# Performance work log

Measured on AMD Instinct MI355X. Metric: run time of the kernel, lower is better.

## Reference

```python
import jax, jax.numpy as jnp
import numpy as np

B, S, LD, Hh, Ww = 64, 32, 16, 32, 18
D, NH, HD, FF, L = 512, 8, 64, 2048, 6
IN = LD * Hh * Ww  # 9216
EPS = 1e-5


def setup_inputs() -> dict:
    key = jax.random.key(0)
    ks = jax.random.split(key, 8)
    p = lambda k, s: jax.random.normal(k, s, jnp.float32) * 0.02
    return {
        "x": jax.random.normal(ks[0], (B, S, LD, Hh, Ww), jnp.float32),
        "inp_w": p(ks[1], (D, IN)), "inp_b": jnp.zeros((D,), jnp.float32),
        "in_proj_w": p(ks[2], (L, 3 * D, D)), "in_proj_b": jnp.zeros((L, 3 * D), jnp.float32),
        "out_w": p(ks[3], (L, D, D)), "out_b": jnp.zeros((L, D), jnp.float32),
        "ln1_w": jnp.ones((L, D), jnp.float32), "ln1_b": jnp.zeros((L, D), jnp.float32),
        "ln2_w": jnp.ones((L, D), jnp.float32), "ln2_b": jnp.zeros((L, D), jnp.float32),
        "ff1_w": p(ks[4], (L, FF, D)), "ff1_b": jnp.zeros((L, FF), jnp.float32),
        "ff2_w": p(ks[5], (L, D, FF)), "ff2_b": jnp.zeros((L, D), jnp.float32),
        "outp_w": p(ks[6], (IN, D)), "outp_b": jnp.zeros((IN,), jnp.float32),
    }


def _layernorm(x, w, b):
    mu = jnp.mean(x, -1, keepdims=True)
    var = jnp.mean(jnp.square(x - mu), -1, keepdims=True)
    return (x - mu) * jax.lax.rsqrt(var + EPS) * w + b


def _rope(x, cos, sin):
    # x: [B,S,NH,HD]; torchtune interleaved-pair rotation, rope applied BEFORE qk projection
    x2 = x.reshape(*x.shape[:-1], HD // 2, 2)
    x0, x1 = x2[..., 0], x2[..., 1]
    c = cos[None, :, None, :]
    s = sin[None, :, None, :]
    out = jnp.stack([x0 * c - x1 * s, x1 * c + x0 * s], axis=-1)
    return out.reshape(x.shape)


def reference(x, inp_w, inp_b, in_proj_w, in_proj_b, out_w, out_b,
              ln1_w, ln1_b, ln2_w, ln2_b, ff1_w, ff1_b, ff2_w, ff2_b,
              outp_w, outp_b):
    b, s = x.shape[0], x.shape[1]
    h = x.reshape(b, s, IN) @ inp_w.T + inp_b  # [B,S,D]

    theta = 1.0 / (10000.0 ** (jnp.arange(0, HD, 2, dtype=jnp.float32) / HD))
    ang = jnp.arange(s, dtype=jnp.float32)[:, None] * theta  # [S, HD/2]
    cos, sin = jnp.cos(ang), jnp.sin(ang)
    mask = jnp.triu(jnp.full((s, s), -jnp.inf, jnp.float32), k=1)  # causal additive mask
    scale = 1.0 / np.sqrt(HD)

    for i in range(L):
        # RoPE on full hidden state (pre-projection), used for q and k; v uses unrotated h
        hr = _rope(h.reshape(b, s, NH, HD), cos, sin).reshape(b, s, D)
        wq, wk, wv = in_proj_w[i, :D], in_proj_w[i, D:2 * D], in_proj_w[i, 2 * D:]
        bq, bk, bv = in_proj_b[i, :D], in_proj_b[i, D:2 * D], in_proj_b[i, 2 * D:]
        q = (hr @ wq.T + bq).reshape(b, s, NH, HD)
        k = (hr @ wk.T + bk).reshape(b, s, NH, HD)
        v = (h @ wv.T + bv).reshape(b, s, NH, HD)
        scores = jnp.einsum('bqhd,bkhd->bhqk', q, k) * scale + mask
        attn = jax.nn.softmax(scores, axis=-1)
        ctx = jnp.einsum('bhqk,bkhd->bqhd', attn, v).reshape(b, s, D)
        sa = ctx @ out_w[i].T + out_b[i]
        h = _layernorm(h + sa, ln1_w[i], ln1_b[i])  # post-norm (norm_first=False)
        ff = jax.nn.gelu(h @ ff1_w[i].T + ff1_b[i], approximate=False) @ ff2_w[i].T + ff2_b[i]
        h = _layernorm(h + ff, ln2_w[i], ln2_b[i])

    out = h @ outp_w.T + outp_b
    return out.reshape(b, s, LD, Hh, Ww)
```

## Files before the change

### kernel.cpp

```cpp
#include <hip/hip_runtime.h>
#include <hip/hip_bf16.h>
#include <math.h>


typedef __attribute__((ext_vector_type(8))) short bf16x8;
typedef __attribute__((ext_vector_type(4))) short bf16x4;
typedef __attribute__((ext_vector_type(8))) float f32x8;
typedef __attribute__((ext_vector_type(4))) float f32x4;

#define LN_EPS 1e-5f

__device__ inline float bf2f(__hip_bfloat16 v) { return __bfloat162float(v); }
__device__ inline __hip_bfloat16 f2bf(float f) { return __float2bfloat16(f); }

__device__ __forceinline__ void gload_lds16(const __hip_bfloat16* g, __hip_bfloat16* l) {
    __builtin_amdgcn_global_load_lds(
        (const __attribute__((address_space(1))) unsigned*)g,
        (__attribute__((address_space(3))) unsigned*)l, 16, 0, 0);
}

__device__ __forceinline__ void sync_tile() {
    asm volatile("s_waitcnt vmcnt(0) lgkmcnt(0)" ::: "memory");
    __builtin_amdgcn_s_barrier();
    asm volatile("" ::: "memory");
}

__device__ __forceinline__ void sync_lds() {
    asm volatile("s_waitcnt lgkmcnt(0)" ::: "memory");
    __builtin_amdgcn_s_barrier();
    asm volatile("" ::: "memory");
}

struct CvtSeg { const float* src; __hip_bfloat16* dst; };
struct CvtArgs { CvtSeg seg[16]; long cum[17]; };

__global__ __launch_bounds__(256) void convert_all(CvtArgs a, long total8,
                                                   float* __restrict__ rtab) {
    if (blockIdx.x == 0) {
#pragma unroll
        for (int it = 0; it < 4; ++it) {
            const int t = it * 256 + threadIdx.x;
            const int s = t >> 5, p = t & 31;
            const float theta = powf(10000.f, -(float)p / 32.f);
            float sn, cs;
            sincosf((float)s * theta, &sn, &cs);
            rtab[t * 2] = cs;
            rtab[t * 2 + 1] = sn;
        }
    }
    const long st = (long)gridDim.x * 256;
    for (long i = (long)blockIdx.x * 256 + threadIdx.x; i < total8; i += 2 * st) {
        int s1 = 0;
        while (i >= a.cum[s1 + 1]) ++s1;
        const long o1 = i - a.cum[s1];
        const f32x8 x1 = *((const f32x8*)a.seg[s1].src + o1);

        const long j = i + st;
        if (j < total8) {
            int s2 = s1;
            while (j >= a.cum[s2 + 1]) ++s2;
            const long o2 = j - a.cum[s2];
            const f32x8 x2 = *((const f32x8*)a.seg[s2].src + o2);

            union { bf16x8 v; __hip_bfloat16 b[8]; } u1, u2;
#pragma unroll
            for (int t = 0; t < 8; ++t) { u1.b[t] = f2bf(x1[t]); u2.b[t] = f2bf(x2[t]); }
            *((bf16x8*)a.seg[s1].dst + o1) = u1.v;
            *((bf16x8*)a.seg[s2].dst + o2) = u2.v;
        } else {
            union { bf16x8 v; __hip_bfloat16 b[8]; } u1;
#pragma unroll
            for (int t = 0; t < 8; ++t) u1.b[t] = f2bf(x1[t]);
            *((bf16x8*)a.seg[s1].dst + o1) = u1.v;
        }
    }
}

template<int BM, int BN, int EPI, int OUT, int AMODE, int SWZ, int PIPE>
__global__ __launch_bounds__(256) void gemm_bt(
    const void* __restrict__ Araw, int bn_split,
    const float* __restrict__ rtab,
    const __hip_bfloat16* __restrict__ W,
    const __hip_bfloat16* __restrict__ bias,
    void* __restrict__ Cv,
    int M, int N, int Ktot, int KC)
{
    constexpr int FM = BM / 32, FN = BN / 32;
    constexpr int CPT_A = BM / 32, CPT_B = BN / 32;
    constexpr bool REGSTAGE = (AMODE == 3 || AMODE == 4);
    constexpr int NBUF = (PIPE && !REGSTAGE) ? 2 : 1;
    __shared__ __align__(16) __hip_bfloat16 sA[NBUF][BM * 64];
    __shared__ __align__(16) __hip_bfloat16 sB[NBUF][BN * 64];

    const int tid = threadIdx.x, lane = tid & 63, wave = tid >> 6;
    const int wr = wave >> 1, wc = wave & 1;
    const int lr = lane & 15, lk = lane >> 4;

    int bm, bn, zz;
    if (SWZ == 0) {
        const int nbm = gridDim.x, nbn = gridDim.y;
        const int nwg = nbm * nbn;
        const int orig = blockIdx.y * nbm + blockIdx.x;
        const int q8 = nwg >> 3, r8 = nwg & 7;
        const int xcd = orig & 7, loc = orig >> 3;
        const int f = (xcd < r8 ? xcd * (q8 + 1) : r8 * (q8 + 1) + (xcd - r8) * q8) + loc;
        bm = f % nbm; bn = f / nbm; zz = blockIdx.z;
    } else {
        const int bid = blockIdx.x;
        const int xcd = bid & 7, loc = bid >> 3;
        const int nbn = N / BN;
        const int per = (gridDim.x >> 3) / nbn;
        bn = loc % nbn;
        const int gid = xcd * per + loc / nbn;
        bm = gid % (M / BM); zz = gid / (M / BM);
    }
    const int kbeg = zz * KC, kend = kbeg + KC;
    const bool dorot = (AMODE == 2 || AMODE == 4) && (bn < bn_split);

    const __hip_bfloat16* Ab = (const __hip_bfloat16*)Araw + (long)bm * BM * Ktot;
    const float*          Af = (const float*)Araw + (long)bm * BM * Ktot;
    const __hip_bfloat16* Wb = W + (long)bn * BN * Ktot;

    f32x4 acc[FM][FN];
#pragma unroll
    for (int i = 0; i < FM; ++i)
#pragma unroll
        for (int j = 0; j < FN; ++j) acc[i][j] = (f32x4){0.f, 0.f, 0.f, 0.f};

    f32x8  aregf[CPT_A];
    bf16x8 aregb[CPT_A];
    f32x8  csreg[CPT_A];
    bf16x8 bregb[REGSTAGE ? CPT_B : 1];

    auto stageA_g = [&](int buf, int k0) {
#pragma unroll
        for (int c = 0; c < CPT_A; ++c) {
            const int ch = tid + c * 256, row = ch >> 3, co = ch & 7;
            gload_lds16(&Ab[(long)row * Ktot + k0 + ((co ^ (row & 7)) * 8)],
                        (__hip_bfloat16*)((char*)&sA[buf][0] + ch * 16));
        }
    };
    auto stageB_g = [&](int buf, int k0) {
#pragma unroll
        for (int c = 0; c < CPT_B; ++c) {
            const int ch = tid + c * 256, row = ch >> 3, co = ch & 7;
            gload_lds16(&Wb[(long)row * Ktot + k0 + ((co ^ (row & 7)) * 8)],
                        (__hip_bfloat16*)((char*)&sB[buf][0] + ch * 16));
        }
    };
    auto issueA = [&](int k0) {
#pragma unroll
        for (int c = 0; c < CPT_A; ++c) {
            const int ch = tid + c * 256, row = ch >> 3, co = ch & 7;
            if (AMODE == 1 || AMODE == 3)
                aregf[c] = *(const f32x8*)&Af[(long)row * Ktot + k0 + co * 8];
            if (AMODE == 2 || AMODE == 4) {
                aregb[c] = *(const bf16x8*)&Ab[(long)row * Ktot + k0 + co * 8];
                if (dorot)
                    csreg[c] = *(const f32x8*)&rtab[((bm * BM + row) & 31) * 64 + co * 8];
            }
        }
        if (REGSTAGE) {
#pragma unroll
            for (int c = 0; c < CPT_B; ++c) {
                const int ch = tid + c * 256, row = ch >> 3, co = ch & 7;
                bregb[c] = *(const bf16x8*)&Wb[(long)row * Ktot + k0 + co * 8];
            }
        }
    };
    auto writeA = [&](int buf) {
#pragma unroll
        for (int c = 0; c < CPT_A; ++c) {
            const int ch = tid + c * 256, row = ch >> 3, co = ch & 7;
            union { bf16x8 v; __hip_bfloat16 b[8]; } t;
            if (AMODE == 1 || AMODE == 3) {
#pragma unroll
                for (int j = 0; j < 8; ++j) t.b[j] = f2bf(aregf[c][j]);
            } else {
                t.v = aregb[c];
                if (dorot) {
#pragma unroll
                    for (int qd = 0; qd < 4; ++qd) {
                        const float c_ = csreg[c][qd * 2], sn = csreg[c][qd * 2 + 1];
                        const float x0 = bf2f(t.b[2 * qd]);
                        const float x1 = bf2f(t.b[2 * qd + 1]);
                        t.b[2 * qd]     = f2bf(x0 * c_ - x1 * sn);
                        t.b[2 * qd + 1] = f2bf(x1 * c_ + x0 * sn);
                    }
                }
            }
            *(bf16x8*)((char*)&sA[buf][0] + row * 128 + ((co ^ (row & 7)) << 4)) = t.v;
        }
        if (REGSTAGE) {
#pragma unroll
            for (int c = 0; c < CPT_B; ++c) {
                const int ch = tid + c * 256, row = ch >> 3, co = ch & 7;
                *(bf16x8*)((char*)&sB[buf][0] + row * 128 + ((co ^ (row & 7)) << 4)) = bregb[c];
            }
        }
    };
    auto compute = [&](int buf) {
        bf16x8 af[2][FM], bfr[2][FN];
#pragma unroll
        for (int ks = 0; ks < 2; ++ks) {
#pragma unroll
            for (int i = 0; i < FM; ++i) {
                const int row = wr * (BM / 2) + i * 16 + lr;
                const int co = ks * 4 + lk;
                af[ks][i] = *(const bf16x8*)((const char*)&sA[buf][0] + row * 128 +
                                             ((co ^ (row & 7)) << 4));
            }
#pragma unroll
            for (int j = 0; j < FN; ++j) {
                const int row = wc * (BN / 2) + j * 16 + lr;
                const int co = ks * 4 + lk;
                bfr[ks][j] = *(const bf16x8*)((const char*)&sB[buf][0] + row * 128 +
                                              ((co ^ (row & 7)) << 4));
            }
        }
#pragma unroll
        for (int ks = 0; ks < 2; ++ks)
#pragma unroll
            for (int i = 0; i < FM; ++i)
#pragma unroll
                for (int j = 0; j < FN; ++j)
                    acc[i][j] = __builtin_amdgcn_mfma_f32_16x16x32_bf16(
                        af[ks][i], bfr[ks][j], acc[i][j], 0, 0, 0);
    };

    if (REGSTAGE) {
        issueA(kbeg);
        for (int k0 = kbeg; k0 < kend; k0 += 64) {
            if (k0 > kbeg) __builtin_amdgcn_s_barrier();
            writeA(0);
            sync_lds();
            if (k0 + 64 < kend) issueA(k0 + 64);
            compute(0);
        }
    } else if (PIPE == 0) {
        if (AMODE != 0) issueA(kbeg);
        for (int k0 = kbeg; k0 < kend; k0 += 64) {
            if (k0 > kbeg) __builtin_amdgcn_s_barrier();
            if (AMODE == 0) stageA_g(0, k0);
            stageB_g(0, k0);
            if (AMODE != 0) writeA(0);
            sync_tile();
            if (AMODE != 0 && k0 + 64 < kend) issueA(k0 + 64);
            compute(0);
        }
    } else {
        if (AMODE == 0) stageA_g(0, kbeg); else issueA(kbeg);
        stageB_g(0, kbeg);
        if (AMODE != 0) writeA(0);
        sync_tile();
        int cur = 0;
        for (int k0 = kbeg; k0 < kend; k0 += 64) {
            const bool hn = (k0 + 64 < kend);
            if (hn) {
                if (AMODE == 0) stageA_g(cur ^ 1, k0 + 64); else issueA(k0 + 64);
                stageB_g(cur ^ 1, k0 + 64);
            }
            compute(cur);
            if (hn) {
                if (AMODE != 0) writeA(cur ^ 1);
                sync_tile();
            }
            cur ^= 1;
        }
    }

    const int row0 = bm * BM + wr * (BM / 2);
    const int col0 = bn * BN + wc * (BN / 2);
    if (OUT == 1) {
        float* Cp = (float*)Cv + (long)zz * M * N;
#pragma unroll
        for (int i = 0; i < FM; ++i)
#pragma unroll
            for (int j = 0; j < FN; ++j) {
                const int col = col0 + j * 16 + lr;
#pragma unroll
                for (int r = 0; r < 4; ++r)
                    Cp[(long)(row0 + i * 16 + lk * 4 + r) * N + col] = acc[i][j][r];
            }
    } else {
#pragma unroll
        for (int i = 0; i < FM; ++i)
#pragma unroll
            for (int j = 0; j < FN; ++j) {
                const int col = col0 + j * 16 + lr;
                const float bv = bf2f(bias[col]);
#pragma unroll
                for (int r = 0; r < 4; ++r) {
                    const int row = row0 + i * 16 + lk * 4 + r;
                    float v = acc[i][j][r] + bv;
                    if (EPI == 1) v = 0.5f * v * (1.0f + erff(v * 0.70710678118654752f));
                    const long idx = (long)row * N + col;
                    if (OUT == 2) ((float*)Cv)[idx] = v;
                    else          ((__hip_bfloat16*)Cv)[idx] = f2bf(v);
                }
            }
    }
}

template<int SK>
__global__ __launch_bounds__(256) void sk_reduce(
    const float* __restrict__ part, const __hip_bfloat16* __restrict__ bias,
    __hip_bfloat16* __restrict__ out)
{
    const long MN = 2048L * 512;
    const long i4 = ((long)blockIdx.x * 256 + threadIdx.x) * 4;
    f32x4 s = (f32x4){0.f, 0.f, 0.f, 0.f};
#pragma unroll
    for (int z = 0; z < SK; ++z) s += *(const f32x4*)&part[z * MN + i4];
    const int col = (int)(i4 & 511);
    union { bf16x4 v; __hip_bfloat16 b[4]; } o;
#pragma unroll
    for (int j = 0; j < 4; ++j) o.b[j] = f2bf(s[j] + bf2f(bias[col + j]));
    *(bf16x4*)&out[i4] = o.v;
}

template<int SK>
__global__ __launch_bounds__(256) void skred_add_ln(
    const float* __restrict__ part, const __hip_bfloat16* __restrict__ bias,
    const __hip_bfloat16* __restrict__ resid,
    const __hip_bfloat16* __restrict__ w, const __hip_bfloat16* __restrict__ b,
    __hip_bfloat16* __restrict__ out)
{
    const long MN = 2048L * 512;
    const int wave = threadIdx.x >> 6, lane = threadIdx.x & 63;
    const long row = (long)blockIdx.x * 4 + wave;
    const long base = row * 512 + lane * 8;

    f32x8 acc = *(const f32x8*)&part[base];
#pragma unroll
    for (int z = 1; z < SK; ++z) acc += *(const f32x8*)&part[z * MN + base];

    union { bf16x8 v; __hip_bfloat16 b[8]; } ur, uo;
    ur.v = *(const bf16x8*)&resid[base];

    float x[8];
    float s = 0.f, s2 = 0.f;
#pragma unroll
    for (int j = 0; j < 8; ++j) {
        const int col = lane * 8 + j;
        x[j] = acc[j] + bf2f(bias[col]) + bf2f(ur.b[j]);
        s += x[j];
        s2 += x[j] * x[j];
    }
#pragma unroll
    for (int off = 32; off; off >>= 1) {
        s  += __shfl_xor(s, off);
        s2 += __shfl_xor(s2, off);
    }
    const float mu = s * (1.f / 512.f);
    const float var = s2 * (1.f / 512.f) - mu * mu;
    const float rs = rsqrtf(var + LN_EPS);
#pragma unroll
    for (int j = 0; j < 8; ++j) {
        const int col = lane * 8 + j;
        uo.b[j] = f2bf((x[j] - mu) * rs * bf2f(w[col]) + bf2f(b[col]));
    }
    *(bf16x8*)&out[base] = uo.v;
}

__global__ __launch_bounds__(256) void attn_mfma(
    const __hip_bfloat16* __restrict__ qkv, __hip_bfloat16* __restrict__ ctx)
{
    __shared__ __align__(16) __hip_bfloat16 sP[4][32 * 32];
    __shared__ __align__(16) __hip_bfloat16 sVT[4][64 * 32];

    const int wave = threadIdx.x >> 6, lane = threadIdx.x & 63;
    const int bh = blockIdx.x * 4 + wave;
    const int b = bh >> 3, head = bh & 7;
    const long tok0 = (long)b * 32;
    const int lr = lane & 15, lk = lane >> 4;

    const __hip_bfloat16* Qb = qkv + tok0 * 1536 + head * 64;
    const __hip_bfloat16* Kb = Qb + 512;
    const __hip_bfloat16* Vb = Qb + 1024;

#pragma unroll
    for (int t = 0; t < 4; ++t) {
        const int c = lane + t * 64, row = c >> 3, d0 = (c & 7) * 8;
        union { bf16x8 v; __hip_bfloat16 e[8]; } u;
        u.v = *(const bf16x8*)&Vb[(long)row * 1536 + d0];
#pragma unroll
        for (int e = 0; e < 8; ++e) sVT[wave][(d0 + e) * 32 + row] = u.e[e];
    }

    f32x4 sc[2][2];
#pragma unroll
    for (int i = 0; i < 2; ++i)
#pragma unroll
        for (int j = 0; j < 2; ++j) sc[i][j] = (f32x4){0.f, 0.f, 0.f, 0.f};
#pragma unroll
    for (int ks = 0; ks < 2; ++ks) {
        bf16x8 aq[2], bk[2];
#pragma unroll
        for (int i = 0; i < 2; ++i)
            aq[i] = *(const bf16x8*)&Qb[(long)(i * 16 + lr) * 1536 + ks * 32 + lk * 8];
#pragma unroll
        for (int j = 0; j < 2; ++j)
            bk[j] = *(const bf16x8*)&Kb[(long)(j * 16 + lr) * 1536 + ks * 32 + lk * 8];
#pragma unroll
        for (int i = 0; i < 2; ++i)
#pragma unroll
            for (int j = 0; j < 2; ++j)
                sc[i][j] = __builtin_amdgcn_mfma_f32_16x16x32_bf16(aq[i], bk[j], sc[i][j], 0, 0, 0);
    }

    float p[2][2][4], inv[2][4];
#pragma unroll
    for (int i = 0; i < 2; ++i) {
#pragma unroll
        for (int r = 0; r < 4; ++r) {
            const int row = i * 16 + lk * 4 + r;
            float m = -3.0e38f;
#pragma unroll
            for (int j = 0; j < 2; ++j) {
                const int col = j * 16 + lr;
                const float v = (col <= row) ? sc[i][j][r] * 0.125f : -3.0e38f;
                p[i][j][r] = v;
                m = fmaxf(m, v);
            }
#pragma unroll
            for (int off = 1; off < 16; off <<= 1)
                m = fmaxf(m, __shfl_xor(m, off));
            float l = 0.f;
#pragma unroll
            for (int j = 0; j < 2; ++j) {
                p[i][j][r] = expf(p[i][j][r] - m);
                l += p[i][j][r];
            }
#pragma unroll
            for (int off = 1; off < 16; off <<= 1)
                l += __shfl_xor(l, off);
            inv[i][r] = 1.f / l;
        }
    }

#pragma unroll
    for (int i = 0; i < 2; ++i)
#pragma unroll
        for (int j = 0; j < 2; ++j)
#pragma unroll
            for (int r = 0; r < 4; ++r)
                sP[wave][(i * 16 + lk * 4 + r) * 32 + j * 16 + lr] = f2bf(p[i][j][r]);

    bf16x8 pa[2], vb[4];
#pragma unroll
    for (int i = 0; i < 2; ++i)
        pa[i] = *(const bf16x8*)&sP[wave][(i * 16 + lr) * 32 + lk * 8];
#pragma unroll
    for (int j = 0; j < 4; ++j)
        vb[j] = *(const bf16x8*)&sVT[wave][(j * 16 + lr) * 32 + lk * 8];

    f32x4 o[2][4];
#pragma unroll
    for (int i = 0; i < 2; ++i)
#pragma unroll
        for (int j = 0; j < 4; ++j) {
            o[i][j] = (f32x4){0.f, 0.f, 0.f, 0.f};
            o[i][j] = __builtin_amdgcn_mfma_f32_16x16x32_bf16(pa[i], vb[j], o[i][j], 0, 0, 0);
        }

#pragma unroll
    for (int i = 0; i < 2; ++i)
#pragma unroll
        for (int j = 0; j < 4; ++j) {
            const int col = j * 16 + lr;
#pragma unroll
            for (int r = 0; r < 4; ++r) {
                const int row = i * 16 + lk * 4 + r;
                ctx[(tok0 + row) * 512 + head * 64 + col] = f2bf(o[i][j][r] * inv[i][r]);
            }
        }
}

extern "C" void kernel_launch(void* const* d_in, const int* in_sizes, int n_in,
                              void* d_out, int out_size, void* d_ws, size_t ws_size,
                              hipStream_t stream)
{
    const int M = 2048;
    __hip_bfloat16* wts = (__hip_bfloat16*)d_ws;

    const long O_INPW   = 0;
    const long O_INPROJ = 4718592;
    const long O_OUTW   = 9437184;
    const long O_FF1    = 11010048;
    const long O_FF2    = 17301504;
    const long O_OUTPW  = 23592960;
    const long O_INPB   = 28311552;
    const long O_INPROJB= 28312064;
    const long O_OUTB   = 28321280;
    const long O_LN1W   = 28324352;
    const long O_LN1B   = 28327424;
    const long O_LN2W   = 28330496;
    const long O_LN2B   = 28333568;
    const long O_FF1B   = 28336640;
    const long O_FF2B   = 28348928;
    const long O_OUTPB  = 28352000;
    const long O_ACT    = 28361216;

    __hip_bfloat16* h   = wts + O_ACT;
    __hip_bfloat16* ht  = h   + (long)M * 512;
    __hip_bfloat16* qkv = ht  + (long)M * 512;
    __hip_bfloat16* ctx = qkv + (long)M * 1536;
    __hip_bfloat16* ffh = ctx + (long)M * 512;
    float* rtab = (float*)(ffh + (long)M * 2048);
    float* skpart = (float*)((__hip_bfloat16*)rtab + 4096);

    const int  cidx[16] = {1, 3, 5, 11, 13, 15, 2, 4, 6, 7, 8, 9, 10, 12, 14, 16};
    const long coff[16] = {O_INPW, O_INPROJ, O_OUTW, O_FF1, O_FF2, O_OUTPW,
                           O_INPB, O_INPROJB, O_OUTB, O_LN1W, O_LN1B, O_LN2W,
                           O_LN2B, O_FF1B, O_FF2B, O_OUTPB};
    const long csz[16]  = {4718592, 4718592, 1572864, 6291456, 6291456, 4718592,
                           512, 9216, 3072, 3072, 3072, 3072, 3072, 12288, 3072, 9216};
    CvtArgs ca;
    long cum = 0;
    for (int s = 0; s < 16; ++s) {
        ca.seg[s].src = (const float*)d_in[cidx[s]];
        ca.seg[s].dst = wts + coff[s];
        ca.cum[s] = cum;
        cum += csz[s] / 8;
    }
    ca.cum[16] = cum;
    convert_all<<<2048, 256, 0, stream>>>(ca, cum, rtab);

    gemm_bt<64, 256, 0, 1, 3, 1, 0><<<512, 256, 0, stream>>>(
        d_in[0], 0, rtab, wts + O_INPW, wts + O_INPB, skpart, M, 512, 9216, 1152);
    sk_reduce<8><<<1024, 256, 0, stream>>>(skpart, wts + O_INPB, h);

    for (int i = 0; i < 6; ++i) {
        const __hip_bfloat16* wqkv = wts + O_INPROJ + (long)i * 1536 * 512;
        const __hip_bfloat16* bqkv = wts + O_INPROJB + i * 1536;

        gemm_bt<64, 128, 0, 0, 4, 0, 0><<<dim3(32, 12), 256, 0, stream>>>(
            h, 8, rtab, wqkv, bqkv, qkv, M, 1536, 512, 512);
        attn_mfma<<<128, 256, 0, stream>>>(qkv, ctx);
        gemm_bt<64, 64, 0, 1, 4, 0, 0><<<dim3(32, 8, 2), 256, 0, stream>>>(
            ctx, 0, rtab, wts + O_OUTW + (long)i * 512 * 512, wts + O_OUTB + i * 512,
            skpart, M, 512, 512, 256);
        skred_add_ln<2><<<512, 256, 0, stream>>>(
            skpart, wts + O_OUTB + i * 512, h,
            wts + O_LN1W + i * 512, wts + O_LN1B + i * 512, ht);
        gemm_bt<64, 128, 1, 0, 4, 0, 0><<<dim3(32, 16), 256, 0, stream>>>(
            ht, 0, rtab, wts + O_FF1 + (long)i * 2048 * 512, wts + O_FF1B + i * 2048,
            ffh, M, 2048, 512, 512);
        gemm_bt<64, 128, 0, 1, 4, 0, 0><<<dim3(32, 4, 4), 256, 0, stream>>>(
            ffh, 0, rtab, wts + O_FF2 + (long)i * 512 * 2048, wts + O_FF2B + i * 512,
            skpart, M, 512, 2048, 512);
        skred_add_ln<4><<<512, 256, 0, stream>>>(
            skpart, wts + O_FF2B + i * 512, ht,
            wts + O_LN2W + i * 512, wts + O_LN2B + i * 512, h);
    }

    gemm_bt<128, 128, 0, 2, 4, 0, 0><<<dim3(16, 72), 256, 0, stream>>>(
        h, 0, rtab, wts + O_OUTPW, wts + O_OUTPB, d_out, M, 9216, 512, 512);
}
```

Before: 458.4 us.

## Overlap remaining weight conversion with input-projection GEMM in one launch

Splits the fp32-to-bf16 weight conversion so that only the input-projection weight, its bias and the RoPE table are converted up front. The other layer weights are converted by extra workgroups appended to a specialized split-K input-projection GEMM kernel, so that conversion traffic runs alongside the large GEMM. The generic GEMM template is also trimmed to its register-staged path, dropping the unused LDS-direct and double-buffer variants. The risk is that the conversion blocks compete with the GEMM for bandwidth and CUs, and the first kernel now does a smaller job.

```diff
diff --git a/kernel.cpp b/kernel.cpp
--- a/kernel.cpp
+++ b/kernel.cpp
@@ -32,10 +32,13 @@
 }
 
 struct CvtSeg { const float* src; __hip_bfloat16* dst; };
-struct CvtArgs { CvtSeg seg[16]; long cum[17]; };
-
-__global__ __launch_bounds__(256) void convert_all(CvtArgs a, long total8,
-                                                   float* __restrict__ rtab) {
+struct CvtArgs14 { CvtSeg seg[14]; long cum[15]; };
+
+__global__ __launch_bounds__(256) void convert_pre(
+    const float* __restrict__ inpw_f, __hip_bfloat16* __restrict__ inpw_b,
+    const float* __restrict__ inpb_f, __hip_bfloat16* __restrict__ inpb_b,
+    float* __restrict__ rtab)
+{
     if (blockIdx.x == 0) {
 #pragma unroll
         for (int it = 0; it < 4; ++it) {
@@ -47,33 +50,176 @@
             rtab[t * 2] = cs;
             rtab[t * 2 + 1] = sn;
         }
-    }
+        if (threadIdx.x < 64) {
+            const long o = threadIdx.x;
+            const f32x8 x = *((const f32x8*)inpb_f + o);
+            union { bf16x8 v; __hip_bfloat16 b[8]; } u;
+#pragma unroll
+            for (int t = 0; t < 8; ++t) u.b[t] = f2bf(x[t]);
+            *((bf16x8*)inpb_b + o) = u.v;
+        }
+    }
+    const long total8 = 4718592 / 8;
     const long st = (long)gridDim.x * 256;
     for (long i = (long)blockIdx.x * 256 + threadIdx.x; i < total8; i += 2 * st) {
-        int s1 = 0;
-        while (i >= a.cum[s1 + 1]) ++s1;
-        const long o1 = i - a.cum[s1];
-        const f32x8 x1 = *((const f32x8*)a.seg[s1].src + o1);
-
+        const f32x8 x1 = *((const f32x8*)inpw_f + i);
         const long j = i + st;
         if (j < total8) {
-            int s2 = s1;
-            while (j >= a.cum[s2 + 1]) ++s2;
-            const long o2 = j - a.cum[s2];
-            const f32x8 x2 = *((const f32x8*)a.seg[s2].src + o2);
-
+            const f32x8 x2 = *((const f32x8*)inpw_f + j);
             union { bf16x8 v; __hip_bfloat16 b[8]; } u1, u2;
 #pragma unroll
             for (int t = 0; t < 8; ++t) { u1.b[t] = f2bf(x1[t]); u2.b[t] = f2bf(x2[t]); }
-            *((bf16x8*)a.seg[s1].dst + o1) = u1.v;
-            *((bf16x8*)a.seg[s2].dst + o2) = u2.v;
+            *((bf16x8*)inpw_b + i) = u1.v;
+            *((bf16x8*)inpw_b + j) = u2.v;
         } else {
             union { bf16x8 v; __hip_bfloat16 b[8]; } u1;
 #pragma unroll
             for (int t = 0; t < 8; ++t) u1.b[t] = f2bf(x1[t]);
-            *((bf16x8*)a.seg[s1].dst + o1) = u1.v;
-        }
-    }
+            *((bf16x8*)inpw_b + i) = u1.v;
+        }
+    }
+}
+
+__global__ __launch_bounds__(256) void inproj_conv(
+    const float* __restrict__ Xf,
+    const __hip_bfloat16* __restrict__ Wall,
+    float* __restrict__ part,
+    CvtArgs14 ca, long total8)
+{
+    __shared__ __align__(16) __hip_bfloat16 sA[64 * 64];
+    __shared__ __align__(16) __hip_bfloat16 sB[256 * 64];
+
+    const int tid = threadIdx.x;
+
+    if (blockIdx.x >= 512) {
+        const long st = 2048L * 256;
+        for (long i = (long)(blockIdx.x - 512) * 256 + tid; i < total8; i += 2 * st) {
+            int s1 = 0;
+            while (i >= ca.cum[s1 + 1]) ++s1;
+            const long o1 = i - ca.cum[s1];
+            const f32x8 x1 = *((const f32x8*)ca.seg[s1].src + o1);
+            const long j = i + st;
+            if (j < total8) {
+                int s2 = s1;
+                while (j >= ca.cum[s2 + 1]) ++s2;
+                const long o2 = j - ca.cum[s2];
+                const f32x8 x2 = *((const f32x8*)ca.seg[s2].src + o2);
+                union { bf16x8 v; __hip_bfloat16 b[8]; } u1, u2;
+#pragma unroll
+                for (int t = 0; t < 8; ++t) { u1.b[t] = f2bf(x1[t]); u2.b[t] = f2bf(x2[t]); }
+                *((bf16x8*)ca.seg[s1].dst + o1) = u1.v;
+                *((bf16x8*)ca.seg[s2].dst + o2) = u2.v;
+            } else {
+                union { bf16x8 v; __hip_bfloat16 b[8]; } u1;
+#pragma unroll
+                for (int t = 0; t < 8; ++t) u1.b[t] = f2bf(x1[t]);
+                *((bf16x8*)ca.seg[s1].dst + o1) = u1.v;
+            }
+        }
+        return;
+    }
+
+    const int lane = tid & 63, wave = tid >> 6;
+    const int wr = wave >> 1, wc = wave & 1;
+    const int lr = lane & 15, lk = lane >> 4;
+
+    const int bid = blockIdx.x;
+    const int xcd = bid & 7, loc = bid >> 3;
+    const int bn = loc & 1;
+    const int gid = xcd * 32 + (loc >> 1);
+    const int bm = gid & 31;
+    const int zz = gid >> 5;
+    const int kbeg = zz * 1152, kend = kbeg + 1152;
+
+    const float* Ab = Xf + (long)bm * 64 * 9216;
+    const __hip_bfloat16* Wb = Wall + (long)bn * 256 * 9216;
+
+    f32x4 acc[2][8];
+#pragma unroll
+    for (int i = 0; i < 2; ++i)
+#pragma unroll
+        for (int j = 0; j < 8; ++j) acc[i][j] = (f32x4){0.f, 0.f, 0.f, 0.f};
+
+    f32x8  aregf[2];
+    bf16x8 bregb[8];
+
+    auto issueA = [&](int k0) {
+#pragma unroll
+        for (int c = 0; c < 2; ++c) {
+            const int ch = tid + c * 256, row = ch >> 3, co = ch & 7;
+            aregf[c] = *(const f32x8*)&Ab[(long)row * 9216 + k0 + co * 8];
+        }
+#pragma unroll
+        for (int c = 0; c < 8; ++c) {
+            const int ch = tid + c * 256, row = ch >> 3, co = ch & 7;
+            bregb[c] = *(const bf16x8*)&Wb[(long)row * 9216 + k0 + co * 8];
+        }
+    };
+    auto writeA = [&]() {
+#pragma unroll
+        for (int c = 0; c < 2; ++c) {
+            const int ch = tid + c * 256, row = ch >> 3, co = ch & 7;
+            union { bf16x8 v; __hip_bfloat16 b[8]; } t;
+#pragma unroll
+            for (int j = 0; j < 8; ++j) t.b[j] = f2bf(aregf[c][j]);
+            *(bf16x8*)((char*)sA + row * 128 + ((co ^ (row & 7)) << 4)) = t.v;
+        }
+#pragma unroll
+        for (int c = 0; c < 8; ++c) {
+            const int ch = tid + c * 256, row = ch >> 3, co = ch & 7;
+            *(bf16x8*)((char*)sB + row * 128 + ((co ^ (row & 7)) << 4)) = bregb[c];
+        }
+    };
+    auto compute = [&]() {
+        bf16x8 af[2][2], bfr[2][8];
+#pragma unroll
+        for (int ks = 0; ks < 2; ++ks) {
+#pragma unroll
+            for (int i = 0; i < 2; ++i) {
+                const int row = wr * 32 + i * 16 + lr;
+                const int co = ks * 4 + lk;
+                af[ks][i] = *(const bf16x8*)((const char*)sA + row * 128 +
+                                             ((co ^ (row & 7)) << 4));
+            }
+#pragma unroll
+            for (int j = 0; j < 8; ++j) {
+                const int row = wc * 128 + j * 16 + lr;
+                const int co = ks * 4 + lk;
+                bfr[ks][j] = *(const bf16x8*)((const char*)sB + row * 128 +
+                                              ((co ^ (row & 7)) << 4));
+            }
+        }
+#pragma unroll
+        for (int ks = 0; ks < 2; ++ks)
+#pragma unroll
+            for (int i = 0; i < 2; ++i)
+#pragma unroll
+                for (int j = 0; j < 8; ++j)
+                    acc[i][j] = __builtin_amdgcn_mfma_f32_16x16x32_bf16(
+                        af[ks][i], bfr[ks][j], acc[i][j], 0, 0, 0);
+    };
+
+    issueA(kbeg);
+    for (int k0 = kbeg; k0 < kend; k0 += 64) {
+        if (k0 > kbeg) __builtin_amdgcn_s_barrier();
+        writeA();
+        sync_lds();
+        if (k0 + 64 < kend) issueA(k0 + 64);
+        compute();
+    }
+
+    float* Cp = part + (long)zz * 2048 * 512;
+    const int row0 = bm * 64 + wr * 32;
+    const int col0 = bn * 256 + wc * 128;
+#pragma unroll
+    for (int i = 0; i < 2; ++i)
+#pragma unroll
+        for (int j = 0; j < 8; ++j) {
+            const int col = col0 + j * 16 + lr;
+#pragma unroll
+            for (int r = 0; r < 4; ++r)
+                Cp[(long)(row0 + i * 16 + lk * 4 + r) * 512 + col] = acc[i][j][r];
+        }
 }
 
 template<int BM, int BN, int EPI, int OUT, int AMODE, int SWZ, int PIPE>
@@ -87,38 +233,25 @@
 {
     constexpr int FM = BM / 32, FN = BN / 32;
     constexpr int CPT_A = BM / 32, CPT_B = BN / 32;
-    constexpr bool REGSTAGE = (AMODE == 3 || AMODE == 4);
-    constexpr int NBUF = (PIPE && !REGSTAGE) ? 2 : 1;
-    __shared__ __align__(16) __hip_bfloat16 sA[NBUF][BM * 64];
-    __shared__ __align__(16) __hip_bfloat16 sB[NBUF][BN * 64];
+    __shared__ __align__(16) __hip_bfloat16 sA[BM * 64];
+    __shared__ __align__(16) __hip_bfloat16 sB[BN * 64];
 
     const int tid = threadIdx.x, lane = tid & 63, wave = tid >> 6;
     const int wr = wave >> 1, wc = wave & 1;
     const int lr = lane & 15, lk = lane >> 4;
 
-    int bm, bn, zz;
-    if (SWZ == 0) {
-        const int nbm = gridDim.x, nbn = gridDim.y;
-        const int nwg = nbm * nbn;
-        const int orig = blockIdx.y * nbm + blockIdx.x;
-        const int q8 = nwg >> 3, r8 = nwg & 7;
-        const int xcd = orig & 7, loc = orig >> 3;
-        const int f = (xcd < r8 ? xcd * (q8 + 1) : r8 * (q8 + 1) + (xcd - r8) * q8) + loc;
-        bm = f % nbm; bn = f / nbm; zz = blockIdx.z;
-    } else {
-        const int bid = blockIdx.x;
-        const int xcd = bid & 7, loc = bid >> 3;
-        const int nbn = N / BN;
-        const int per = (gridDim.x >> 3) / nbn;
-        bn = loc % nbn;
-        const int gid = xcd * per + loc / nbn;
-        bm = gid % (M / BM); zz = gid / (M / BM);
-    }
+    const int nbm = gridDim.x, nbn = gridDim.y;
+    const int nwg = nbm * nbn;
+    const int orig = blockIdx.y * nbm + blockIdx.x;
+    const int q8 = nwg >> 3, r8 = nwg & 7;
+    const int xcd = orig & 7, loc = orig >> 3;
+    const int f = (xcd < r8 ? xcd * (q8 + 1) : r8 * (q8 + 1) + (xcd - r8) * q8) + loc;
+    const int bm = f % nbm, bn = f / nbm;
+    const int zz = blockIdx.z;
     const int kbeg = zz * KC, kend = kbeg + KC;
-    const bool dorot = (AMODE == 2 || AMODE == 4) && (bn < bn_split);
+    const bool dorot = (AMODE == 4) && (bn < bn_split);
 
     const __hip_bfloat16* Ab = (const __hip_bfloat16*)Araw + (long)bm * BM * Ktot;
-    const float*          Af = (const float*)Araw + (long)bm * BM * Ktot;
     const __hip_bfloat16* Wb = W + (long)bn * BN * Ktot;
 
     f32x4 acc[FM][FN];
@@ -127,79 +260,49 @@
 #pragma unroll
         for (int j = 0; j < FN; ++j) acc[i][j] = (f32x4){0.f, 0.f, 0.f, 0.f};
 
-    f32x8  aregf[CPT_A];
     bf16x8 aregb[CPT_A];
     f32x8  csreg[CPT_A];
-    bf16x8 bregb[REGSTAGE ? CPT_B : 1];
-
-    auto stageA_g = [&](int buf, int k0) {
+    bf16x8 bregb[CPT_B];
+
+    auto issueA = [&](int k0) {
 #pragma unroll
         for (int c = 0; c < CPT_A; ++c) {
             const int ch = tid + c * 256, row = ch >> 3, co = ch & 7;
-            gload_lds16(&Ab[(long)row * Ktot + k0 + ((co ^ (row & 7)) * 8)],
-                        (__hip_bfloat16*)((char*)&sA[buf][0] + ch * 16));
+            aregb[c] = *(const bf16x8*)&Ab[(long)row * Ktot + k0 + co * 8];
+            if (dorot)
+                csreg[c] = *(const f32x8*)&rtab[((bm * BM + row) & 31) * 64 + co * 8];
+        }
+#pragma unroll
+        for (int c = 0; c < CPT_B; ++c) {
+            const int ch = tid + c * 256, row = ch >> 3, co = ch & 7;
+            bregb[c] = *(const bf16x8*)&Wb[(long)row * Ktot + k0 + co * 8];
         }
     };
-    auto stageB_g = [&](int buf, int k0) {
+    auto writeA = [&]() {
+#pragma unroll
+        for (int c = 0; c < CPT_A; ++c) {
+            const int ch = tid + c * 256, row = ch >> 3, co = ch & 7;
+            union { bf16x8 v; __hip_bfloat16 b[8]; } t;
+            t.v = aregb[c];
+            if (dorot) {
+#pragma unroll
+                for (int qd = 0; qd < 4; ++qd) {
+                    const float c_ = csreg[c][qd * 2], sn = csreg[c][qd * 2 + 1];
+                    const float x0 = bf2f(t.b[2 * qd]);
+                    const float x1 = bf2f(t.b[2 * qd + 1]);
+                    t.b[2 * qd]     = f2bf(x0 * c_ - x1 * sn);
+                    t.b[2 * qd + 1] = f2bf(x1 * c_ + x0 * sn);
+                }
+            }
+            *(bf16x8*)((char*)sA + row * 128 + ((co ^ (row & 7)) << 4)) = t.v;
+        }
 #pragma unroll
         for (int c = 0; c < CPT_B; ++c) {
             const int ch = tid + c * 256, row = ch >> 3, co = ch & 7;
-            gload_lds16(&Wb[(long)row * Ktot + k0 + ((co ^ (row & 7)) * 8)],
-                        (__hip_bfloat16*)((char*)&sB[buf][0] + ch * 16));
+            *(bf16x8*)((char*)sB + row * 128 + ((co ^ (row & 7)) << 4)) = bregb[c];
         }
     };
-    auto issueA = [&](int k0) {
-#pragma unroll
-        for (int c = 0; c < CPT_A; ++c) {
-            const int ch = tid + c * 256, row = ch >> 3, co = ch & 7;
-            if (AMODE == 1 || AMODE == 3)
-                aregf[c] = *(const f32x8*)&Af[(long)row * Ktot + k0 + co * 8];
-            if (AMODE == 2 || AMODE == 4) {
-                aregb[c] = *(const bf16x8*)&Ab[(long)row * Ktot + k0 + co * 8];
-                if (dorot)
-                    csreg[c] = *(const f32x8*)&rtab[((bm * BM + row) & 31) * 64 + co * 8];
-            }
-        }
-        if (REGSTAGE) {
-#pragma unroll
-            for (int c = 0; c < CPT_B; ++c) {
-                const int ch = tid + c * 256, row = ch >> 3, co = ch & 7;
-                bregb[c] = *(const bf16x8*)&Wb[(long)row * Ktot + k0 + co * 8];
-            }
-        }
-    };
-    auto writeA = [&](int buf) {
-#pragma unroll
-        for (int c = 0; c < CPT_A; ++c) {
-            const int ch = tid + c * 256, row = ch >> 3, co = ch & 7;
-            union { bf16x8 v; __hip_bfloat16 b[8]; } t;
-            if (AMODE == 1 || AMODE == 3) {
-#pragma unroll
-                for (int j = 0; j < 8; ++j) t.b[j] = f2bf(aregf[c][j]);
-            } else {
-                t.v = aregb[c];
-                if (dorot) {
-#pragma unroll
-                    for (int qd = 0; qd < 4; ++qd) {
-                        const float c_ = csreg[c][qd * 2], sn = csreg[c][qd * 2 + 1];
-                        const float x0 = bf2f(t.b[2 * qd]);
-                        const float x1 = bf2f(t.b[2 * qd + 1]);
-                        t.b[2 * qd]     = f2bf(x0 * c_ - x1 * sn);
-                        t.b[2 * qd + 1] = f2bf(x1 * c_ + x0 * sn);
-                    }
-                }
-            }
-            *(bf16x8*)((char*)&sA[buf][0] + row * 128 + ((co ^ (row & 7)) << 4)) = t.v;
-        }
-        if (REGSTAGE) {
-#pragma unroll
-            for (int c = 0; c < CPT_B; ++c) {
-                const int ch = tid + c * 256, row = ch >> 3, co = ch & 7;
-                *(bf16x8*)((char*)&sB[buf][0] + row * 128 + ((co ^ (row & 7)) << 4)) = bregb[c];
-            }
-        }
-    };
-    auto compute = [&](int buf) {
+    auto compute = [&]() {
         bf16x8 af[2][FM], bfr[2][FN];
 #pragma unroll
         for (int ks = 0; ks < 2; ++ks) {
@@ -207,14 +310,14 @@
             for (int i = 0; i < FM; ++i) {
                 const int row = wr * (BM / 2) + i * 16 + lr;
                 const int co = ks * 4 + lk;
-                af[ks][i] = *(const bf16x8*)((const char*)&sA[buf][0] + row * 128 +
+                af[ks][i] = *(const bf16x8*)((const char*)sA + row * 128 +
                                              ((co ^ (row & 7)) << 4));
             }
 #pragma unroll
             for (int j = 0; j < FN; ++j) {
                 const int row = wc * (BN / 2) + j * 16 + lr;
                 const int co = ks * 4 + lk;
-                bfr[ks][j] = *(const bf16x8*)((const char*)&sB[buf][0] + row * 128 +
+                bfr[ks][j] = *(const bf16x8*)((const char*)sB + row * 128 +
                                               ((co ^ (row & 7)) << 4));
             }
         }
@@ -228,45 +331,13 @@
                         af[ks][i], bfr[ks][j], acc[i][j], 0, 0, 0);
     };
 
-    if (REGSTAGE) {
-        issueA(kbeg);
-        for (int k0 = kbeg; k0 < kend; k0 += 64) {
-            if (k0 > kbeg) __builtin_amdgcn_s_barrier();
-            writeA(0);
-            sync_lds();
-            if (k0 + 64 < kend) issueA(k0 + 64);
-            compute(0);
-        }
-    } else if (PIPE == 0) {
-        if (AMODE != 0) issueA(kbeg);
-        for (int k0 = kbeg; k0 < kend; k0 += 64) {
-            if (k0 > kbeg) __builtin_amdgcn_s_barrier();
-            if (AMODE == 0) stageA_g(0, k0);
-            stageB_g(0, k0);
-            if (AMODE != 0) writeA(0);
-            sync_tile();
-            if (AMODE != 0 && k0 + 64 < kend) issueA(k0 + 64);
-            compute(0);
-        }
-    } else {
-        if (AMODE == 0) stageA_g(0, kbeg); else issueA(kbeg);
-        stageB_g(0, kbeg);
-        if (AMODE != 0) writeA(0);
-        sync_tile();
-        int cur = 0;
-        for (int k0 = kbeg; k0 < kend; k0 += 64) {
-            const bool hn = (k0 + 64 < kend);
-            if (hn) {
-                if (AMODE == 0) stageA_g(cur ^ 1, k0 + 64); else issueA(k0 + 64);
-                stageB_g(cur ^ 1, k0 + 64);
-            }
-            compute(cur);
-            if (hn) {
-                if (AMODE != 0) writeA(cur ^ 1);
-                sync_tile();
-            }
-            cur ^= 1;
-        }
+    issueA(kbeg);
+    for (int k0 = kbeg; k0 < kend; k0 += 64) {
+        if (k0 > kbeg) __builtin_amdgcn_s_barrier();
+        writeA();
+        sync_lds();
+        if (k0 + 64 < kend) issueA(k0 + 64);
+        compute();
     }
 
     const int row0 = bm * BM + wr * (BM / 2);
@@ -510,25 +581,28 @@
     float* rtab = (float*)(ffh + (long)M * 2048);
     float* skpart = (float*)((__hip_bfloat16*)rtab + 4096);
 
-    const int  cidx[16] = {1, 3, 5, 11, 13, 15, 2, 4, 6, 7, 8, 9, 10, 12, 14, 16};
-    const long coff[16] = {O_INPW, O_INPROJ, O_OUTW, O_FF1, O_FF2, O_OUTPW,
-                           O_INPB, O_INPROJB, O_OUTB, O_LN1W, O_LN1B, O_LN2W,
+    const int  cidx[14] = {3, 5, 11, 13, 15, 4, 6, 7, 8, 9, 10, 12, 14, 16};
+    const long coff[14] = {O_INPROJ, O_OUTW, O_FF1, O_FF2, O_OUTPW,
+                           O_INPROJB, O_OUTB, O_LN1W, O_LN1B, O_LN2W,
                            O_LN2B, O_FF1B, O_FF2B, O_OUTPB};
-    const long csz[16]  = {4718592, 4718592, 1572864, 6291456, 6291456, 4718592,
-                           512, 9216, 3072, 3072, 3072, 3072, 3072, 12288, 3072, 9216};
-    CvtArgs ca;
+    const long csz[14]  = {4718592, 1572864, 6291456, 6291456, 4718592,
+                           9216, 3072, 3072, 3072, 3072, 3072, 12288, 3072, 9216};
+    CvtArgs14 ca;
     long cum = 0;
-    for (int s = 0; s < 16; ++s) {
+    for (int s = 0; s < 14; ++s) {
         ca.seg[s].src = (const float*)d_in[cidx[s]];
         ca.seg[s].dst = wts + coff[s];
         ca.cum[s] = cum;
         cum += csz[s] / 8;
     }
-    ca.cum[16] = cum;
-    convert_all<<<2048, 256, 0, stream>>>(ca, cum, rtab);
-
-    gemm_bt<64, 256, 0, 1, 3, 1, 0><<<512, 256, 0, stream>>>(
-        d_in[0], 0, rtab, wts + O_INPW, wts + O_INPB, skpart, M, 512, 9216, 1152);
+    ca.cum[14] = cum;
+
+    convert_pre<<<1024, 256, 0, stream>>>(
+        (const float*)d_in[1], wts + O_INPW,
+        (const float*)d_in[2], wts + O_INPB, rtab);
+
+    inproj_conv<<<2560, 256, 0, stream>>>(
+        (const float*)d_in[0], wts + O_INPW, skpart, ca, cum);
     sk_reduce<8><<<1024, 256, 0, stream>>>(skpart, wts + O_INPB, h);
 
     for (int i = 0; i < 6; ++i) {
```

Measured after the change: 469.2 us. 2.4% more time.
